# Performance work log

Hardware: AMD Instinct MI355X
Metric: run time of the kernel (lower is better)

## Reference

```python
import jax, jax.numpy as jnp
import numpy as np

N = 16384
K = 4096  # codebook_size
D = 512   # embedding_dim
COMMITMENT_COST = 0.25


def setup_inputs() -> dict:
    key = jax.random.key(0)
    kz, kc = jax.random.split(key)
    z = jax.random.normal(kz, (N, D), dtype=jnp.float32)
    # nn.Embedding weight init: uniform(-1/K, 1/K)
    codebook = jax.random.uniform(kc, (K, D), dtype=jnp.float32,
                                  minval=-1.0 / K, maxval=1.0 / K)
    return {"z": z, "codebook": codebook}


def reference(z, codebook):
    # squared L2 distances: [N, K]
    dists = (jnp.sum(z * z, axis=1, keepdims=True)
             + jnp.sum(codebook * codebook, axis=1)
             - 2.0 * jnp.matmul(z, codebook.T))
    idx = jnp.argmin(dists, axis=1)                 # [N]
    z_q = codebook[idx]                             # gather == one-hot @ codebook
    # straight-through estimator
    z_q_ste = z + jax.lax.stop_gradient(z_q - z)
    commitment_loss = jnp.mean((jax.lax.stop_gradient(z) - z_q) ** 2)
    codebook_loss = jnp.mean((z - jax.lax.stop_gradient(z_q)) ** 2)
    loss = codebook_loss + COMMITMENT_COST * commitment_loss
    encoding_indices = idx[:, None]                 # [N, 1] to match torch shape
    return (z_q_ste, encoding_indices, loss)
```

## Files before the change

### kernel.cpp

```cpp
#include <hip/hip_runtime.h>
#include <math.h>

#define N_ROWS 16384
#define K_CODES 4096
#define D_DIM 512
#define NCHUNK 8
#define KCHUNK (K_CODES / NCHUNK)
#define MARGIN 2.5e-3f

typedef unsigned int uint32;
typedef unsigned short u16t;
typedef __attribute__((ext_vector_type(8))) short short8;
typedef __attribute__((ext_vector_type(4))) float f32x4;

__device__ __forceinline__ float fmul_(float a, float b) { return __fmul_rn(a, b); }
__device__ __forceinline__ float fadd_(float a, float b) { return __fadd_rn(a, b); }

__device__ __forceinline__ u16t f2bf(float x) {
    uint32 u = __float_as_uint(x);
    return (u16t)((u + 0x7fffu + ((u >> 16) & 1u)) >> 16);
}
__device__ __forceinline__ float bf2f(u16t b) {
    return __uint_as_float(((uint32)b) << 16);
}

__global__ void rownorm_np_kernel(const float* __restrict__ src, int nrows,
                                  float* __restrict__ out) {
    int gid = blockIdx.x * blockDim.x + threadIdx.x;
    int row = gid >> 2;
    int blk = gid & 3;
    if (row >= nrows) return;
    const float4* p = (const float4*)(src + (size_t)row * D_DIM + blk * 128);
    float4 v0 = p[0], v1 = p[1];
    float r0 = fmul_(v0.x, v0.x), r1 = fmul_(v0.y, v0.y);
    float r2 = fmul_(v0.z, v0.z), r3 = fmul_(v0.w, v0.w);
    float r4 = fmul_(v1.x, v1.x), r5 = fmul_(v1.y, v1.y);
    float r6 = fmul_(v1.z, v1.z), r7 = fmul_(v1.w, v1.w);
#pragma unroll
    for (int i = 1; i < 16; i++) {
        float4 w0 = p[2 * i], w1 = p[2 * i + 1];
        r0 = fadd_(r0, fmul_(w0.x, w0.x));
        r1 = fadd_(r1, fmul_(w0.y, w0.y));
        r2 = fadd_(r2, fmul_(w0.z, w0.z));
        r3 = fadd_(r3, fmul_(w0.w, w0.w));
        r4 = fadd_(r4, fmul_(w1.x, w1.x));
        r5 = fadd_(r5, fmul_(w1.y, w1.y));
        r6 = fadd_(r6, fmul_(w1.z, w1.z));
        r7 = fadd_(r7, fmul_(w1.w, w1.w));
    }
    float s = fadd_(fadd_(fadd_(r0, r1), fadd_(r2, r3)),
                    fadd_(fadd_(r4, r5), fadd_(r6, r7)));
    float u = __shfl_down(s, 1, 64);
    float t = fadd_(s, u);
    float w = __shfl_down(t, 2, 64);
    float tot = fadd_(t, w);
    if (blk == 0) out[row] = tot;
}

__global__ void cvt_bf16_kernel(const float* __restrict__ src,
                                u16t* __restrict__ dst, int n4) {
    int i = blockIdx.x * blockDim.x + threadIdx.x;
    if (i >= n4) return;
    float4 v = ((const float4*)src)[i];
    ushort4 o;
    o.x = f2bf(v.x); o.y = f2bf(v.y); o.z = f2bf(v.z); o.w = f2bf(v.w);
    ((ushort4*)dst)[i] = o;
}

#define STS 136

__global__ __launch_bounds__(256) void score_gemm_kernel(
    const u16t* __restrict__ zb, const u16t* __restrict__ cbb,
    const float* __restrict__ cnorm, u16t* __restrict__ scores) {
    __shared__ alignas(16) u16t Ab[128 * 32];
    __shared__ alignas(16) u16t Bb[128 * 32];
    __shared__ alignas(16) u16t stile[128 * STS];

    const int t = threadIdx.x;
    const int bx = blockIdx.x;
    const int by = blockIdx.y;
    const int row0 = by * 128, k0 = bx * KCHUNK;
    const int w = t >> 6, lane = t & 63;
    const int wx = w & 1, wy = w >> 1;
    const int l15 = lane & 15, quad = lane >> 4;

    for (int kt = 0; kt < 4; kt++) {
        f32x4 acc[4][4];
#pragma unroll
        for (int i = 0; i < 4; i++)
#pragma unroll
            for (int j = 0; j < 4; j++) acc[i][j] = (f32x4){0.f, 0.f, 0.f, 0.f};

        for (int dt = 0; dt < 16; dt++) {
            __syncthreads();
#pragma unroll
            for (int q = 0; q < 2; q++) {
                int s = q * 256 + t;
                const u16t* ga = zb + (size_t)(row0 + (s >> 2)) * D_DIM + dt * 32 + (s & 3) * 8;
                __builtin_amdgcn_global_load_lds(
                    (const __attribute__((address_space(1))) void*)ga,
                    (__attribute__((address_space(3))) void*)((char*)Ab + q * 4096 + w * 1024),
                    16, 0, 0);
                const u16t* gb = cbb + (size_t)(k0 + kt * 128 + (s >> 2)) * D_DIM + dt * 32 + (s & 3) * 8;
                __builtin_amdgcn_global_load_lds(
                    (const __attribute__((address_space(1))) void*)gb,
                    (__attribute__((address_space(3))) void*)((char*)Bb + q * 4096 + w * 1024),
                    16, 0, 0);
            }
            __syncthreads();
            short8 a[4], b[4];
#pragma unroll
            for (int i = 0; i < 4; i++)
                a[i] = *(const short8*)((char*)Ab + (wy * 64 + i * 16 + l15) * 64 + quad * 16);
#pragma unroll
            for (int j = 0; j < 4; j++)
                b[j] = *(const short8*)((char*)Bb + (wx * 64 + j * 16 + l15) * 64 + quad * 16);
#pragma unroll
            for (int i = 0; i < 4; i++)
#pragma unroll
                for (int j = 0; j < 4; j++)
                    acc[i][j] = __builtin_amdgcn_mfma_f32_16x16x32_bf16(a[i], b[j], acc[i][j], 0, 0, 0);
        }
#pragma unroll
        for (int j = 0; j < 4; j++) {
            int cl = wx * 64 + j * 16 + l15;
            float cn = cnorm[k0 + kt * 128 + cl];
#pragma unroll
            for (int i = 0; i < 4; i++) {
#pragma unroll
                for (int r = 0; r < 4; r++) {
                    int rl = wy * 64 + i * 16 + quad * 4 + r;
                    float s = fmaf(-2.f, acc[i][j][r], cn);
                    stile[rl * STS + cl] = f2bf(s);
                }
            }
        }
        __syncthreads();
        for (int idx = t; idx < 128 * 16; idx += 256) {
            int row = idx >> 4, seg = idx & 15;
            short8 v = *(const short8*)&stile[row * STS + seg * 8];
            *(short8*)(scores + (size_t)(row0 + row) * K_CODES + k0 + kt * 128 + seg * 8) = v;
        }
    }
}

__global__ __launch_bounds__(256) void scan_refine_wave_kernel(
    const u16t* __restrict__ scores,
    const float* __restrict__ z, const float* __restrict__ cb,
    const float* __restrict__ zz, const float* __restrict__ cnorm,
    float* __restrict__ out_zq, float* __restrict__ out_idx,
    float* __restrict__ rowsum) {
    const int t = threadIdx.x;
    const int w = t >> 6, lane = t & 63;
    const int row = blockIdx.x * 4 + w;

    const u16t* srow = scores + (size_t)row * K_CODES;
    short8 sv[8];
#pragma unroll
    for (int p = 0; p < 8; p++)
        sv[p] = *(const short8*)(srow + p * 512 + lane * 8);

    float m = 3.4e38f;
#pragma unroll
    for (int p = 0; p < 8; p++)
#pragma unroll
        for (int e = 0; e < 8; e++)
            m = fminf(m, bf2f((u16t)sv[p][e]));
#pragma unroll
    for (int off = 1; off < 64; off <<= 1)
        m = fminf(m, __shfl_xor(m, off, 64));
    const float thr = m + MARGIN;

    const float* zr = z + (size_t)row * D_DIM;
    float4 z0 = *(const float4*)(zr + lane * 8);
    float4 z1 = *(const float4*)(zr + lane * 8 + 4);
    const float zzr = zz[row];

    float bv = 3.4e38f;
    int bi = 0x7fffffff;
#pragma unroll
    for (int p = 0; p < 8; p++) {
        uint32 lm = 0u;
#pragma unroll
        for (int e = 0; e < 8; e++)
            if (bf2f((u16t)sv[p][e]) <= thr) lm |= (1u << e);
        unsigned long long act = __ballot(lm != 0u);
        while (act) {
            int src = __ffsll(act) - 1;
            act &= act - 1;
            uint32 mb = (uint32)__shfl((int)lm, src, 64);
            while (mb) {
                int e = __ffs(mb) - 1;
                mb &= mb - 1;
                int k = p * 512 + src * 8 + e;
                const float* cr = cb + (size_t)k * D_DIM;
                float4 c0 = *(const float4*)(cr + lane * 8);
                float4 c1 = *(const float4*)(cr + lane * 8 + 4);
                float d = fmul_(z0.x, c0.x);
                d = fmaf(z0.y, c0.y, d); d = fmaf(z0.z, c0.z, d); d = fmaf(z0.w, c0.w, d);
                d = fmaf(z1.x, c1.x, d); d = fmaf(z1.y, c1.y, d);
                d = fmaf(z1.z, c1.z, d); d = fmaf(z1.w, c1.w, d);
#pragma unroll
                for (int off = 1; off < 64; off <<= 1)
                    d = fadd_(d, __shfl_xor(d, off, 64));
                float dist = fmaf(-2.f, d, fadd_(zzr, cnorm[k]));
                if (dist < bv || (dist == bv && k < bi)) { bv = dist; bi = k; }
            }
        }
    }
    const float* cq = cb + (size_t)bi * D_DIM;
    float4 c0 = *(const float4*)(cq + lane * 8);
    float4 c1 = *(const float4*)(cq + lane * 8 + 4);
    float4 o0, o1;
    o0.x = fadd_(z0.x, __fsub_rn(c0.x, z0.x));
    o0.y = fadd_(z0.y, __fsub_rn(c0.y, z0.y));
    o0.z = fadd_(z0.z, __fsub_rn(c0.z, z0.z));
    o0.w = fadd_(z0.w, __fsub_rn(c0.w, z0.w));
    o1.x = fadd_(z1.x, __fsub_rn(c1.x, z1.x));
    o1.y = fadd_(z1.y, __fsub_rn(c1.y, z1.y));
    o1.z = fadd_(z1.z, __fsub_rn(c1.z, z1.z));
    o1.w = fadd_(z1.w, __fsub_rn(c1.w, z1.w));
    float* orow = out_zq + (size_t)row * D_DIM + lane * 8;
    *(float4*)(orow) = o0;
    *(float4*)(orow + 4) = o1;
    float dx0 = z0.x - c0.x, dy0 = z0.y - c0.y, dz0 = z0.z - c0.z, dw0 = z0.w - c0.w;
    float dx1 = z1.x - c1.x, dy1 = z1.y - c1.y, dz1 = z1.z - c1.z, dw1 = z1.w - c1.w;
    float s = dx0 * dx0 + dy0 * dy0 + dz0 * dz0 + dw0 * dw0
            + dx1 * dx1 + dy1 * dy1 + dz1 * dz1 + dw1 * dw1;
#pragma unroll
    for (int off = 32; off; off >>= 1) s += __shfl_down(s, off, 64);
    if (lane == 0) {
        rowsum[row] = s;
        out_idx[row] = (float)bi;
    }
}

__global__ void loss_kernel(const float* __restrict__ rowsum,
                            float* __restrict__ out_loss) {
    __shared__ float sm[256];
    float s = 0.f;
    for (int i = threadIdx.x; i < N_ROWS; i += 256) s += rowsum[i];
    sm[threadIdx.x] = s;
    __syncthreads();
    for (int st = 128; st; st >>= 1) {
        if (threadIdx.x < st) sm[threadIdx.x] += sm[threadIdx.x + st];
        __syncthreads();
    }
    if (threadIdx.x == 0)
        *out_loss = 1.25f * sm[0] / (float)(N_ROWS * D_DIM);
}

#define BM 128
#define BN 128
#define BK 16
#define TM 8
#define TN 8

__global__ __launch_bounds__(256, 4) void vq_argmin_kernel(
    const float* __restrict__ z, const float* __restrict__ cb,
    const float* __restrict__ zz, const float* __restrict__ cnorm,
    float* __restrict__ pval, int* __restrict__ pidx) {
    __shared__ float As[BK][BM + 4];
    __shared__ float Bs[BK][BN + 4];
    __shared__ float rv[BM][17];
    __shared__ int   ri[BM][17];

    const int bx = blockIdx.x;
    const int by = blockIdx.y;
    const int row0 = by * BM;
    const int k0 = bx * KCHUNK;
    const int t = threadIdx.x;
    const int tx = t & 15;
    const int ty = t >> 4;

    float minv[TM];
    int   mini[TM];
#pragma unroll
    for (int i = 0; i < TM; i++) { minv[i] = 3.4e38f; mini[i] = 0; }
    float zrow[TM];
#pragma unroll
    for (int i = 0; i < TM; i++) zrow[i] = zz[row0 + ty * TM + i];
    const int sr = t >> 1;
    const int sdq = (t & 1) * 8;

    for (int kt = 0; kt < KCHUNK / BN; kt++) {
        const int col0 = k0 + kt * BN;
        float acc[TM][TN];
#pragma unroll
        for (int i = 0; i < TM; i++)
#pragma unroll
            for (int j = 0; j < TN; j++) acc[i][j] = 0.f;
        for (int dt = 0; dt < D_DIM; dt += BK) {
            {
                const float* src = z + (size_t)(row0 + sr) * D_DIM + dt + sdq;
                float4 v0 = *(const float4*)(src);
                float4 v1 = *(const float4*)(src + 4);
                As[sdq + 0][sr] = v0.x; As[sdq + 1][sr] = v0.y;
                As[sdq + 2][sr] = v0.z; As[sdq + 3][sr] = v0.w;
                As[sdq + 4][sr] = v1.x; As[sdq + 5][sr] = v1.y;
                As[sdq + 6][sr] = v1.z; As[sdq + 7][sr] = v1.w;
                const float* srcb = cb + (size_t)(col0 + sr) * D_DIM + dt + sdq;
                float4 w0 = *(const float4*)(srcb);
                float4 w1 = *(const float4*)(srcb + 4);
                Bs[sdq + 0][sr] = w0.x; Bs[sdq + 1][sr] = w0.y;
                Bs[sdq + 2][sr] = w0.z; Bs[sdq + 3][sr] = w0.w;
                Bs[sdq + 4][sr] = w1.x; Bs[sdq + 5][sr] = w1.y;
                Bs[sdq + 6][sr] = w1.z; Bs[sdq + 7][sr] = w1.w;
            }
            __syncthreads();
#pragma unroll
            for (int d = 0; d < BK; d++) {
                float a[TM], b[TN];
#pragma unroll
                for (int i = 0; i < TM; i++) a[i] = As[d][ty * TM + i];
#pragma unroll
                for (int j = 0; j < TN; j++) b[j] = Bs[d][tx * TN + j];
#pragma unroll
                for (int i = 0; i < TM; i++)
#pragma unroll
                    for (int j = 0; j < TN; j++)
                        acc[i][j] = fmaf(a[i], b[j], acc[i][j]);
            }
            __syncthreads();
        }
#pragma unroll
        for (int j = 0; j < TN; j++) {
            const int col = col0 + tx * TN + j;
            const float cn = cnorm[col];
#pragma unroll
            for (int i = 0; i < TM; i++) {
                float s1 = fadd_(zrow[i], cn);
                float s = fmaf(-2.f, acc[i][j], s1);
                if (s < minv[i]) { minv[i] = s; mini[i] = col; }
            }
        }
    }
#pragma unroll
    for (int i = 0; i < TM; i++) {
        rv[ty * TM + i][tx] = minv[i];
        ri[ty * TM + i][tx] = mini[i];
    }
    __syncthreads();
    if (t < BM) {
        float bv = rv[t][0];
        int   bi = ri[t][0];
#pragma unroll
        for (int x = 1; x < 16; x++) {
            float v = rv[t][x]; int ii = ri[t][x];
            if (v < bv || (v == bv && ii < bi)) { bv = v; bi = ii; }
        }
        pval[(size_t)(row0 + t) * NCHUNK + bx] = bv;
        pidx[(size_t)(row0 + t) * NCHUNK + bx] = bi;
    }
}

__global__ void finalize_kernel(const float* __restrict__ z,
                                const float* __restrict__ cb,
                                const float* __restrict__ pval,
                                const int* __restrict__ pidx,
                                float* __restrict__ out_zq,
                                float* __restrict__ out_idx,
                                float* __restrict__ rowsum) {
    int row = (blockIdx.x * blockDim.x + threadIdx.x) >> 6;
    int lane = threadIdx.x & 63;
    if (row >= N_ROWS) return;
    float bv = pval[(size_t)row * NCHUNK];
    int   bi = pidx[(size_t)row * NCHUNK];
#pragma unroll
    for (int c = 1; c < NCHUNK; c++) {
        float v = pval[(size_t)row * NCHUNK + c];
        int  ii = pidx[(size_t)row * NCHUNK + c];
        if (v < bv || (v == bv && ii < bi)) { bv = v; bi = ii; }
    }
    const float4* zr = (const float4*)(z + (size_t)row * D_DIM);
    const float4* cr = (const float4*)(cb + (size_t)bi * D_DIM);
    float4* orow = (float4*)(out_zq + (size_t)row * D_DIM);
    float s = 0.f;
#pragma unroll
    for (int i = 0; i < 2; i++) {
        float4 zv = zr[i * 64 + lane];
        float4 cv = cr[i * 64 + lane];
        float4 o;
        o.x = fadd_(zv.x, __fsub_rn(cv.x, zv.x));
        o.y = fadd_(zv.y, __fsub_rn(cv.y, zv.y));
        o.z = fadd_(zv.z, __fsub_rn(cv.z, zv.z));
        o.w = fadd_(zv.w, __fsub_rn(cv.w, zv.w));
        orow[i * 64 + lane] = o;
        float dx = zv.x - cv.x, dy = zv.y - cv.y;
        float dz = zv.z - cv.z, dw = zv.w - cv.w;
        s += dx * dx + dy * dy + dz * dz + dw * dw;
    }
#pragma unroll
    for (int off = 32; off; off >>= 1) s += __shfl_down(s, off, 64);
    if (lane == 0) {
        rowsum[row] = s;
        out_idx[row] = (float)bi;
    }
}

extern "C" void kernel_launch(void* const* d_in, const int* in_sizes, int n_in,
                              void* d_out, int out_size, void* d_ws, size_t ws_size,
                              hipStream_t stream) {
    const float* z  = (const float*)d_in[0];
    const float* cb = (const float*)d_in[1];
    float* out      = (float*)d_out;
    float* out_zq   = out;
    float* out_idx  = out + (size_t)N_ROWS * D_DIM;
    float* out_loss = out_idx + N_ROWS;

    float* zz     = (float*)d_ws;
    float* cnorm  = zz + N_ROWS;
    float* rowsum = cnorm + K_CODES;
    u16t*  z_bf   = (u16t*)(rowsum + N_ROWS);
    u16t*  cb_bf  = z_bf + (size_t)N_ROWS * D_DIM;
    u16t*  scores = cb_bf + (size_t)K_CODES * D_DIM;
    const size_t WS_NEEDED = (size_t)(N_ROWS + K_CODES + N_ROWS) * 4
                           + (size_t)N_ROWS * D_DIM * 2
                           + (size_t)K_CODES * D_DIM * 2
                           + (size_t)N_ROWS * K_CODES * 2;

    if (ws_size >= WS_NEEDED) {
        cvt_bf16_kernel<<<(N_ROWS * D_DIM / 4) / 256, 256, 0, stream>>>(z, z_bf, N_ROWS * D_DIM / 4);
        cvt_bf16_kernel<<<(K_CODES * D_DIM / 4) / 256, 256, 0, stream>>>(cb, cb_bf, K_CODES * D_DIM / 4);
        rownorm_np_kernel<<<(N_ROWS * 4) / 256, 256, 0, stream>>>(z, N_ROWS, zz);
        rownorm_np_kernel<<<(K_CODES * 4) / 256, 256, 0, stream>>>(cb, K_CODES, cnorm);

        dim3 g1(NCHUNK, N_ROWS / 128);
        score_gemm_kernel<<<g1, 256, 0, stream>>>(z_bf, cb_bf, cnorm, scores);
        scan_refine_wave_kernel<<<N_ROWS / 4, 256, 0, stream>>>(scores, z, cb, zz, cnorm,
                                                                out_zq, out_idx, rowsum);
        loss_kernel<<<1, 256, 0, stream>>>(rowsum, out_loss);
    } else {
        float* pval = rowsum + N_ROWS;
        int*   pidx = (int*)(pval + (size_t)N_ROWS * NCHUNK);
        rownorm_np_kernel<<<(N_ROWS * 4) / 256, 256, 0, stream>>>(z, N_ROWS, zz);
        rownorm_np_kernel<<<(K_CODES * 4) / 256, 256, 0, stream>>>(cb, K_CODES, cnorm);
        dim3 g2(NCHUNK, N_ROWS / BM);
        vq_argmin_kernel<<<g2, 256, 0, stream>>>(z, cb, zz, cnorm, pval, pidx);
        finalize_kernel<<<N_ROWS / 4, 256, 0, stream>>>(z, cb, pval, pidx,
                                                        out_zq, out_idx, rowsum);
        loss_kernel<<<1, 256, 0, stream>>>(rowsum, out_loss);
    }
}
```

Before: 291.4 us.

## Emit per-tile row minima from GEMM and scan only candidate score tiles

The score GEMM now computes each row's minimum score per 128-code tile in fp32 and writes it to a small workspace array. The refine kernel reads these 32 tile minima to form its threshold and loads bf16 scores only for tiles whose minimum is within the margin, instead of streaming the whole 4096-entry score row. This removes most of the score-row reads in the scan kernel at the cost of extra shuffles and reductions in the GEMM epilogue plus one more small global write. The threshold is now based on the fp32 minimum rather than the bf16-rounded one, so the candidate set can differ slightly, and the best index is masked to stay in range.

```diff
diff --git a/kernel.cpp b/kernel.cpp
--- a/kernel.cpp
+++ b/kernel.cpp
@@ -6,6 +6,7 @@
 #define D_DIM 512
 #define NCHUNK 8
 #define KCHUNK (K_CODES / NCHUNK)
+#define N_TILES 32
 #define MARGIN 2.5e-3f
 
 typedef unsigned int uint32;
@@ -71,10 +72,12 @@
 
 __global__ __launch_bounds__(256) void score_gemm_kernel(
     const u16t* __restrict__ zb, const u16t* __restrict__ cbb,
-    const float* __restrict__ cnorm, u16t* __restrict__ scores) {
+    const float* __restrict__ cnorm, u16t* __restrict__ scores,
+    float* __restrict__ pmin_g) {
     __shared__ alignas(16) u16t Ab[128 * 32];
     __shared__ alignas(16) u16t Bb[128 * 32];
     __shared__ alignas(16) u16t stile[128 * STS];
+    __shared__ float rmin2[2][128];
 
     const int t = threadIdx.x;
     const int bx = blockIdx.x;
@@ -121,16 +124,41 @@
                 for (int j = 0; j < 4; j++)
                     acc[i][j] = __builtin_amdgcn_mfma_f32_16x16x32_bf16(a[i], b[j], acc[i][j], 0, 0, 0);
         }
+        float cn[4];
+#pragma unroll
+        for (int j = 0; j < 4; j++)
+            cn[j] = cnorm[k0 + kt * 128 + wx * 64 + j * 16 + l15];
+
+        float rm[16];
+#pragma unroll
+        for (int i = 0; i < 4; i++)
+#pragma unroll
+            for (int r = 0; r < 4; r++) {
+                float m = 3.4e38f;
+#pragma unroll
+                for (int j = 0; j < 4; j++)
+                    m = fminf(m, fmaf(-2.f, acc[i][j][r], cn[j]));
+                rm[i * 4 + r] = m;
+            }
+#pragma unroll
+        for (int off = 1; off < 16; off <<= 1)
+#pragma unroll
+            for (int p = 0; p < 16; p++)
+                rm[p] = fminf(rm[p], __shfl_xor(rm[p], off, 64));
+        if (l15 == 0) {
+#pragma unroll
+            for (int p = 0; p < 16; p++)
+                rmin2[wx][wy * 64 + (p >> 2) * 16 + quad * 4 + (p & 3)] = rm[p];
+        }
 #pragma unroll
         for (int j = 0; j < 4; j++) {
             int cl = wx * 64 + j * 16 + l15;
-            float cn = cnorm[k0 + kt * 128 + cl];
 #pragma unroll
             for (int i = 0; i < 4; i++) {
 #pragma unroll
                 for (int r = 0; r < 4; r++) {
                     int rl = wy * 64 + i * 16 + quad * 4 + r;
-                    float s = fmaf(-2.f, acc[i][j][r], cn);
+                    float s = fmaf(-2.f, acc[i][j][r], cn[j]);
                     stile[rl * STS + cl] = f2bf(s);
                 }
             }
@@ -141,11 +169,14 @@
             short8 v = *(const short8*)&stile[row * STS + seg * 8];
             *(short8*)(scores + (size_t)(row0 + row) * K_CODES + k0 + kt * 128 + seg * 8) = v;
         }
-    }
-}
-
-__global__ __launch_bounds__(256) void scan_refine_wave_kernel(
-    const u16t* __restrict__ scores,
+        if (t < 128)
+            pmin_g[(size_t)(row0 + t) * N_TILES + bx * 4 + kt] =
+                fminf(rmin2[0][t], rmin2[1][t]);
+    }
+}
+
+__global__ __launch_bounds__(256) void scan_refine_pmin_kernel(
+    const u16t* __restrict__ scores, const float* __restrict__ pmin_g,
     const float* __restrict__ z, const float* __restrict__ cb,
     const float* __restrict__ zz, const float* __restrict__ cnorm,
     float* __restrict__ out_zq, float* __restrict__ out_idx,
@@ -154,22 +185,12 @@
     const int w = t >> 6, lane = t & 63;
     const int row = blockIdx.x * 4 + w;
 
-    const u16t* srow = scores + (size_t)row * K_CODES;
-    short8 sv[8];
-#pragma unroll
-    for (int p = 0; p < 8; p++)
-        sv[p] = *(const short8*)(srow + p * 512 + lane * 8);
-
-    float m = 3.4e38f;
-#pragma unroll
-    for (int p = 0; p < 8; p++)
-#pragma unroll
-        for (int e = 0; e < 8; e++)
-            m = fminf(m, bf2f((u16t)sv[p][e]));
+    float pm = (lane < N_TILES) ? pmin_g[(size_t)row * N_TILES + lane] : 3.4e38f;
+    float gm = pm;
 #pragma unroll
     for (int off = 1; off < 64; off <<= 1)
-        m = fminf(m, __shfl_xor(m, off, 64));
-    const float thr = m + MARGIN;
+        gm = fminf(gm, __shfl_xor(gm, off, 64));
+    const float thr = gm + MARGIN;
 
     const float* zr = z + (size_t)row * D_DIM;
     float4 z0 = *(const float4*)(zr + lane * 8);
@@ -178,12 +199,14 @@
 
     float bv = 3.4e38f;
     int bi = 0x7fffffff;
-#pragma unroll
-    for (int p = 0; p < 8; p++) {
-        uint32 lm = 0u;
-#pragma unroll
-        for (int e = 0; e < 8; e++)
-            if (bf2f((u16t)sv[p][e]) <= thr) lm |= (1u << e);
+
+    for (int ti = 0; ti < N_TILES; ti++) {
+        float pmv = __shfl(pm, ti, 64);
+        if (pmv > thr) continue;
+        uint32 sw = *(const uint32*)(scores + (size_t)row * K_CODES + ti * 128 + lane * 2);
+        float s0 = bf2f((u16t)(sw & 0xffffu));
+        float s1 = bf2f((u16t)(sw >> 16));
+        uint32 lm = (s0 <= thr ? 1u : 0u) | (s1 <= thr ? 2u : 0u);
         unsigned long long act = __ballot(lm != 0u);
         while (act) {
             int src = __ffsll(act) - 1;
@@ -192,7 +215,7 @@
             while (mb) {
                 int e = __ffs(mb) - 1;
                 mb &= mb - 1;
-                int k = p * 512 + src * 8 + e;
+                int k = ti * 128 + src * 2 + e;
                 const float* cr = cb + (size_t)k * D_DIM;
                 float4 c0 = *(const float4*)(cr + lane * 8);
                 float4 c1 = *(const float4*)(cr + lane * 8 + 4);
@@ -208,6 +231,7 @@
             }
         }
     }
+    bi &= (K_CODES - 1);
     const float* cq = cb + (size_t)bi * D_DIM;
     float4 c0 = *(const float4*)(cq + lane * 8);
     float4 c1 = *(const float4*)(cq + lane * 8 + 4);
@@ -414,10 +438,12 @@
     u16t*  z_bf   = (u16t*)(rowsum + N_ROWS);
     u16t*  cb_bf  = z_bf + (size_t)N_ROWS * D_DIM;
     u16t*  scores = cb_bf + (size_t)K_CODES * D_DIM;
+    float* pmin_g = (float*)(scores + (size_t)N_ROWS * K_CODES);
     const size_t WS_NEEDED = (size_t)(N_ROWS + K_CODES + N_ROWS) * 4
                            + (size_t)N_ROWS * D_DIM * 2
                            + (size_t)K_CODES * D_DIM * 2
-                           + (size_t)N_ROWS * K_CODES * 2;
+                           + (size_t)N_ROWS * K_CODES * 2
+                           + (size_t)N_ROWS * N_TILES * 4;
 
     if (ws_size >= WS_NEEDED) {
         cvt_bf16_kernel<<<(N_ROWS * D_DIM / 4) / 256, 256, 0, stream>>>(z, z_bf, N_ROWS * D_DIM / 4);
@@ -426,8 +452,9 @@
         rownorm_np_kernel<<<(K_CODES * 4) / 256, 256, 0, stream>>>(cb, K_CODES, cnorm);
 
         dim3 g1(NCHUNK, N_ROWS / 128);
-        score_gemm_kernel<<<g1, 256, 0, stream>>>(z_bf, cb_bf, cnorm, scores);
-        scan_refine_wave_kernel<<<N_ROWS / 4, 256, 0, stream>>>(scores, z, cb, zz, cnorm,
+        score_gemm_kernel<<<g1, 256, 0, stream>>>(z_bf, cb_bf, cnorm, scores, pmin_g);
+        scan_refine_pmin_kernel<<<N_ROWS / 4, 256, 0, stream>>>(scores, pmin_g,
+                                                                z, cb, zz, cnorm,
                                                                 out_zq, out_idx, rowsum);
         loss_kernel<<<1, 256, 0, stream>>>(rowsum, out_loss);
     } else {
```

Measured after the change: 293.0 us. Within noise of the previous version (+0.5%).
